# Performance work log

Measured on AMD Instinct MI355X. Metric: run time of the kernel, lower is better.

Reference implementation:

```python
import jax, jax.numpy as jnp
import numpy as np

HIDDEN = 128
EDGE = 64
EPS = 1e-5

def setup_inputs() -> dict:
    key = jax.random.key(0)
    ks = jax.random.split(key, 12)
    B, N, D = 8, 256, HIDDEN
    h = jax.random.normal(ks[0], (B, N, D), dtype=jnp.float32)
    edge_feats = jax.random.normal(ks[1], (B, N, N, 3), dtype=jnp.float32)
    adj_mask = jax.random.bernoulli(ks[2], 0.5, (B, N, N))
    s = lambda fan_in: 1.0 / np.sqrt(fan_in)
    W1 = jax.random.uniform(ks[3], (D + 3, EDGE), minval=-s(D + 3), maxval=s(D + 3))
    b1 = jnp.zeros((EDGE,), jnp.float32)
    W2 = jax.random.uniform(ks[4], (EDGE, D), minval=-s(EDGE), maxval=s(EDGE))
    b2 = jnp.zeros((D,), jnp.float32)
    U1 = jax.random.uniform(ks[5], (3 * D, D), minval=-s(3 * D), maxval=s(3 * D))
    b3 = jnp.zeros((D,), jnp.float32)
    U2 = jax.random.uniform(ks[6], (D, D), minval=-s(D), maxval=s(D))
    b4 = jnp.zeros((D,), jnp.float32)
    gamma = jnp.ones((D,), jnp.float32)
    beta = jnp.zeros((D,), jnp.float32)
    return {"h": h, "edge_feats": edge_feats, "adj_mask": adj_mask,
            "W1": W1, "b1": b1, "W2": W2, "b2": b2,
            "U1": U1, "b3": b3, "U2": U2, "b4": b4,
            "gamma": gamma, "beta": beta}

def reference(h, edge_feats, adj_mask, W1, b1, W2, b2, U1, b3, U2, b4, gamma, beta):
    B, N, D = h.shape
    # NOTE: torch does h.unsqueeze(2).expand(B,N,N,D): h_j[b,i,j,:] = h[b,i,:]
    h_j = jnp.broadcast_to(h[:, :, None, :], (B, N, N, D))
    gate_in = jnp.concatenate([h_j, edge_feats], axis=-1)          # (B,N,N,D+3)
    gates = jax.nn.sigmoid(jax.nn.relu(gate_in @ W1 + b1) @ W2 + b2)  # (B,N,N,D)
    mask_f = adj_mask.astype(h.dtype)[..., None]                    # (B,N,N,1)
    messages = gates * h_j * mask_f
    neighbor_count = jnp.clip(jnp.sum(mask_f, axis=2), 1.0)         # (B,N,1)
    agg_mean = jnp.sum(messages, axis=2) / neighbor_count           # (B,N,D)
    msgs_max = jnp.where(adj_mask[..., None], messages, -jnp.inf)
    agg_max = jnp.max(msgs_max, axis=2)
    agg_max = jnp.where(jnp.isinf(agg_max), 0.0, agg_max)
    upd_in = jnp.concatenate([h, agg_mean, agg_max], axis=-1)       # (B,N,3D)
    upd = jax.nn.relu(upd_in @ U1 + b3) @ U2 + b4
    x = h + upd
    mu = jnp.mean(x, axis=-1, keepdims=True)
    var = jnp.var(x, axis=-1, keepdims=True)
    return (x - mu) * jax.lax.rsqrt(var + EPS) * gamma + beta
```

## Files before the change

kernel.cpp:

```cpp
#include <hip/hip_runtime.h>
#include <hip/hip_bf16.h>
#include <math.h>

#define NN 256
#define DD 128
#define EE 64
#define APAD 392
#define RPAD 136

typedef __attribute__((ext_vector_type(8))) short short8;
typedef __attribute__((ext_vector_type(4))) float f32x4;

static __device__ __forceinline__ unsigned short f2bf(float f) {
    __hip_bfloat16 b = __float2bfloat16(f);
    return *reinterpret_cast<unsigned short*>(&b);
}

static __device__ __forceinline__ float sigm(float l) {
    return __fdividef(1.f, 1.f + __expf(-l));
}

static __device__ __forceinline__ short8 ldb(const float* __restrict__ B, int kbase, int d) {
    unsigned short tmp[8];
    #pragma unroll
    for (int j = 0; j < 8; ++j) tmp[j] = f2bf(B[(kbase + j) * DD + d]);
    return *(const short8*)tmp;
}

__global__ __launch_bounds__(256, 4)
void ecgc_gate(const float* __restrict__ h_g,
               const float* __restrict__ ef_g,
               const int*   __restrict__ mask_g,
               const float* __restrict__ W1_g,
               const float* __restrict__ b1_g,
               const float* __restrict__ W2_g,
               const float* __restrict__ b2_g,
               const float* __restrict__ U1_g,
               const float* __restrict__ U2_g,
               float*          __restrict__ aggf,
               unsigned short* __restrict__ u1t,
               unsigned short* __restrict__ u2t)
{
    const int bi   = blockIdx.x;
    const int t    = threadIdx.x;
    const int lane = t & 63;
    const int w    = t >> 6;
    const int m16  = lane & 15;
    const int quad = lane >> 4;

    __shared__ __align__(16) float sh_ef4[NN * 4];
    __shared__ __align__(16) float sh_q4[EE * 4];
    __shared__ float sh_basep[4 * EE];
    __shared__ float sh_w1e[3 * EE];
    __shared__ int   sh_jlist[NN], sh_wcnt[4], sh_cnt;

    if (t < 32) {
        const int flat = bi * 32 + t;
        if (flat < 384 * DD) {
            const int d = flat / 384, k = flat - d * 384;
            u1t[flat] = f2bf(U1_g[k * DD + d]);
        } else {
            const int f2i = flat - 384 * DD;
            const int d = f2i >> 7, k = f2i & 127;
            u2t[f2i] = f2bf(U2_g[k * DD + d]);
        }
    }

    {
        const float* efr = ef_g + (size_t)bi * NN * 3;
        sh_ef4[t * 4 + 0] = efr[t * 3 + 0];
        sh_ef4[t * 4 + 1] = efr[t * 3 + 1];
        sh_ef4[t * 4 + 2] = efr[t * 3 + 2];
        sh_ef4[t * 4 + 3] = 0.f;
    }
    if (t < 192) sh_w1e[t] = W1_g[(DD + (t >> 6)) * EE + (t & 63)];

    const int mk = (mask_g[bi * NN + t] != 0) ? 1 : 0;
    const unsigned long long bal = __ballot(mk);
    if (lane == 0) sh_wcnt[w] = __popcll(bal);
    const int pre = __popcll(bal & ((1ull << lane) - 1ull));

    {
        const int e = t & 63;
        float acc = 0.f;
        #pragma unroll 8
        for (int d = w * 32; d < w * 32 + 32; ++d)
            acc = fmaf(h_g[bi * DD + d], W1_g[d * EE + e], acc);
        sh_basep[w * EE + e] = acc;
    }

    const int dstripe = w * 32;
    short8 bfrag[2][2];
    float  nb2[2], hd2[2], flip[2];
    #pragma unroll
    for (int dt = 0; dt < 2; ++dt) {
        const int d = dstripe + 16 * dt + m16;
        nb2[dt] = b2_g[d];
        hd2[dt] = h_g[bi * DD + d];
        flip[dt] = (hd2[dt] >= 0.f) ? 1.f : -1.f;
        #pragma unroll
        for (int kh = 0; kh < 2; ++kh)
            bfrag[dt][kh] = ldb(W2_g, kh * 32 + quad * 8, d);
    }
    __syncthreads();

    {
        int wbase = 0;
        for (int ww = 0; ww < w; ++ww) wbase += sh_wcnt[ww];
        if (mk) sh_jlist[wbase + pre] = t;
        if (t == 0) sh_cnt = sh_wcnt[0] + sh_wcnt[1] + sh_wcnt[2] + sh_wcnt[3];
    }
    if (t < EE) {
        const float base = b1_g[t] + sh_basep[t] + sh_basep[EE + t] +
                           sh_basep[2 * EE + t] + sh_basep[3 * EE + t];
        sh_q4[t * 4 + 0] = base;
        sh_q4[t * 4 + 1] = sh_w1e[t];
        sh_q4[t * 4 + 2] = sh_w1e[EE + t];
        sh_q4[t * 4 + 3] = sh_w1e[2 * EE + t];
    }
    __syncthreads();

    f32x4 qa[8], qb[8];
    #pragma unroll
    for (int jj = 0; jj < 8; ++jj) {
        qa[jj] = *(const f32x4*)&sh_q4[(quad * 8 + jj) * 4];
        qb[jj] = *(const f32x4*)&sh_q4[(32 + quad * 8 + jj) * 4];
    }

    const int cnt = sh_cnt;
    const int njt = (cnt + 15) >> 4;

    float sum2[2] = {0.f, 0.f};
    float mm[2]   = {-3.0e38f, -3.0e38f};

    for (int jt = 0; jt < njt; ++jt) {
        const int row = jt * 16 + m16;
        int jl = sh_jlist[row];
        jl = (row < cnt) ? jl : 0;
        const float4 efv = *(const float4*)&sh_ef4[jl * 4];

        union { short8 s; __hip_bfloat162 h2[4]; } ua, ub;
        #pragma unroll
        for (int p = 0; p < 4; ++p) {
            const f32x4 qa0 = qa[2 * p], qa1 = qa[2 * p + 1];
            const f32x4 qb0 = qb[2 * p], qb1 = qb[2 * p + 1];
            float2 va, vb;
            va.x = fmaxf(fmaf(efv.z, qa0[3], fmaf(efv.y, qa0[2], fmaf(efv.x, qa0[1], qa0[0]))), 0.f);
            va.y = fmaxf(fmaf(efv.z, qa1[3], fmaf(efv.y, qa1[2], fmaf(efv.x, qa1[1], qa1[0]))), 0.f);
            vb.x = fmaxf(fmaf(efv.z, qb0[3], fmaf(efv.y, qb0[2], fmaf(efv.x, qb0[1], qb0[0]))), 0.f);
            vb.y = fmaxf(fmaf(efv.z, qb1[3], fmaf(efv.y, qb1[2], fmaf(efv.x, qb1[1], qb1[0]))), 0.f);
            ua.h2[p] = __float22bfloat162_rn(va);
            ub.h2[p] = __float22bfloat162_rn(vb);
        }

        const bool tail = (jt == njt - 1) && (cnt & 15);
        #pragma unroll
        for (int dt = 0; dt < 2; ++dt) {
            f32x4 acc = {nb2[dt], nb2[dt], nb2[dt], nb2[dt]};
            acc = __builtin_amdgcn_mfma_f32_16x16x32_bf16(ua.s, bfrag[dt][0], acc, 0, 0, 0);
            acc = __builtin_amdgcn_mfma_f32_16x16x32_bf16(ub.s, bfrag[dt][1], acc, 0, 0, 0);
            if (!tail) {
                #pragma unroll
                for (int r = 0; r < 4; ++r) {
                    const float l = acc[r];
                    mm[dt] = fmaxf(mm[dt], l * flip[dt]);
                    sum2[dt] += sigm(l);
                }
            } else {
                #pragma unroll
                for (int r = 0; r < 4; ++r) {
                    const bool v = (jt * 16 + quad * 4 + r) < cnt;
                    const float lx = v ? acc[r] : -3.0e38f;
                    const float pf = v ? acc[r] * flip[dt] : -3.0e38f;
                    mm[dt] = fmaxf(mm[dt], pf);
                    sum2[dt] += sigm(lx);
                }
            }
        }
    }

    #pragma unroll
    for (int dt = 0; dt < 2; ++dt) {
        float s = sum2[dt], M = mm[dt];
        s += __shfl_xor(s, 16, 64);  s += __shfl_xor(s, 32, 64);
        M  = fmaxf(M,  __shfl_xor(M, 16, 64));  M  = fmaxf(M,  __shfl_xor(M, 32, 64));
        if (quad == 0) {
            const int d = dstripe + 16 * dt + m16;
            const float hd = hd2[dt];
            float mean = 0.f, amax = 0.f;
            if (cnt > 0) {
                mean = hd * s * __fdividef(1.f, (float)cnt);
                amax = hd * sigm(flip[dt] * M);
            }
            aggf[bi * 256 + d]       = mean;
            aggf[bi * 256 + 128 + d] = amax;
        }
    }
}

__global__ __launch_bounds__(256, 2)
void ecgc_upd(const float* __restrict__ h_g,
              const float* __restrict__ aggf,
              const unsigned short* __restrict__ u1t,
              const unsigned short* __restrict__ u2t,
              const float* __restrict__ b3_g,
              const float* __restrict__ b4_g,
              const float* __restrict__ gam_g,
              const float* __restrict__ bet_g,
              float*       __restrict__ out_g)
{
    const int bi0  = blockIdx.x * 16;
    const int t    = threadIdx.x;
    const int lane = t & 63;
    const int w    = t >> 6;
    const int m16  = lane & 15;
    const int quad = lane >> 4;

    __shared__ __align__(16) unsigned short shA[16 * APAD];
    __shared__ __align__(16) unsigned short rbuf[16 * RPAD];
    __shared__ float sh_s[4 * 16], sh_s2[4 * 16], sh_mu[16], sh_rs[16];

    {
        const int row = t >> 4, q = t & 15;
        const float* hrow = h_g  + (size_t)(bi0 + row) * DD;
        const float* wrow = aggf + (size_t)(bi0 + row) * 256;
        unsigned short tmp[24];
        #pragma unroll
        for (int c = 0; c < 24; ++c) {
            const int col = q * 24 + c;
            float v;
            if (col < 128)      v = hrow[col];
            else if (col < 256) v = wrow[col - 128];
            else                v = wrow[col - 256 + 128];
            tmp[c] = f2bf(v);
        }
        #pragma unroll
        for (int s8 = 0; s8 < 3; ++s8)
            *(short8*)&shA[row * APAD + q * 24 + s8 * 8] = *(const short8*)&tmp[s8 * 8];
    }
    __syncthreads();

    const int dstripe = w * 32;

    f32x4 acc[2];
    #pragma unroll
    for (int dt = 0; dt < 2; ++dt) {
        const float bb = b3_g[dstripe + dt * 16 + m16];
        acc[dt] = (f32x4){bb, bb, bb, bb};
    }
    for (int kk = 0; kk < 12; ++kk) {
        const short8 a0 = *(const short8*)&shA[m16 * APAD + kk * 32 + quad * 8];
        #pragma unroll
        for (int dt = 0; dt < 2; ++dt) {
            const int d = dstripe + dt * 16 + m16;
            const short8 b = *(const short8*)&u1t[(size_t)d * 384 + kk * 32 + quad * 8];
            acc[dt] = __builtin_amdgcn_mfma_f32_16x16x32_bf16(a0, b, acc[dt], 0, 0, 0);
        }
    }

    #pragma unroll
    for (int dt = 0; dt < 2; ++dt) {
        const int d = dstripe + dt * 16 + m16;
        #pragma unroll
        for (int r = 0; r < 4; ++r) {
            const int ro = quad * 4 + r;
            rbuf[ro * RPAD + d] = f2bf(fmaxf(acc[dt][r], 0.f));
        }
    }
    __syncthreads();

    f32x4 acc2[2];
    #pragma unroll
    for (int dt = 0; dt < 2; ++dt) {
        const float bb = b4_g[dstripe + dt * 16 + m16];
        acc2[dt] = (f32x4){bb, bb, bb, bb};
    }
    for (int kk = 0; kk < 4; ++kk) {
        const short8 a0 = *(const short8*)&rbuf[m16 * RPAD + kk * 32 + quad * 8];
        #pragma unroll
        for (int dt = 0; dt < 2; ++dt) {
            const int d = dstripe + dt * 16 + m16;
            const short8 b = *(const short8*)&u2t[(size_t)d * 128 + kk * 32 + quad * 8];
            acc2[dt] = __builtin_amdgcn_mfma_f32_16x16x32_bf16(a0, b, acc2[dt], 0, 0, 0);
        }
    }

    float xv[2][4];
    #pragma unroll
    for (int dt = 0; dt < 2; ++dt) {
        const int d = dstripe + dt * 16 + m16;
        #pragma unroll
        for (int r = 0; r < 4; ++r) {
            const int ro = quad * 4 + r;
            xv[dt][r] = h_g[(size_t)(bi0 + ro) * DD + d] + acc2[dt][r];
        }
    }

    #pragma unroll
    for (int r = 0; r < 4; ++r) {
        float s  = xv[0][r] + xv[1][r];
        float s2 = xv[0][r] * xv[0][r] + xv[1][r] * xv[1][r];
        #pragma unroll
        for (int off = 1; off < 16; off <<= 1) {
            s  += __shfl_xor(s,  off, 64);
            s2 += __shfl_xor(s2, off, 64);
        }
        if (m16 == 0) {
            const int ro = quad * 4 + r;
            sh_s[w * 16 + ro]  = s;
            sh_s2[w * 16 + ro] = s2;
        }
    }
    __syncthreads();
    if (t < 16) {
        const float S  = sh_s[t]  + sh_s[16 + t]  + sh_s[32 + t]  + sh_s[48 + t];
        const float S2 = sh_s2[t] + sh_s2[16 + t] + sh_s2[32 + t] + sh_s2[48 + t];
        const float mu  = S * (1.f / 128.f);
        const float var = S2 * (1.f / 128.f) - mu * mu;
        sh_mu[t] = mu;
        sh_rs[t] = rsqrtf(var + 1e-5f);
    }
    __syncthreads();

    #pragma unroll
    for (int dt = 0; dt < 2; ++dt) {
        const int d = dstripe + dt * 16 + m16;
        const float ga = gam_g[d], be = bet_g[d];
        #pragma unroll
        for (int r = 0; r < 4; ++r) {
            const int ro = quad * 4 + r;
            out_g[(size_t)(bi0 + ro) * DD + d] =
                (xv[dt][r] - sh_mu[ro]) * sh_rs[ro] * ga + be;
        }
    }
}

extern "C" void kernel_launch(void* const* d_in, const int* in_sizes, int n_in,
                              void* d_out, int out_size, void* d_ws, size_t ws_size,
                              hipStream_t stream) {
    float* aggf = (float*)d_ws;
    unsigned short* u1t = (unsigned short*)((char*)d_ws + (size_t)2048 * 256 * 4);
    unsigned short* u2t = u1t + 384 * DD;
    ecgc_gate<<<8 * NN, 256, 0, stream>>>(
        (const float*)d_in[0],
        (const float*)d_in[1],
        (const int*)d_in[2],
        (const float*)d_in[3],
        (const float*)d_in[4],
        (const float*)d_in[5],
        (const float*)d_in[6],
        (const float*)d_in[7],
        (const float*)d_in[9],
        aggf, u1t, u2t);
    ecgc_upd<<<(8 * NN) / 16, 256, 0, stream>>>(
        (const float*)d_in[0],
        aggf, u1t, u2t,
        (const float*)d_in[8],
        (const float*)d_in[10],
        (const float*)d_in[11],
        (const float*)d_in[12],
        (float*)d_out);
}
```

Measured before the change: 121.7 us.

## Process two node rows per gate block to amortize setup and W2 fragment loads

Each gate block now handles two (batch,node) rows instead of one, halving the grid size. The per-block setup is shared across both rows: the W2 bf16 fragment loads, the W1 edge weights and the W1 column reads for the base projection. Edge features, masks and compacted neighbor lists are staged in LDS for both rows, and the neighbor loop then runs twice. The aim is to cut redundant global loads and launch overhead per row. In exchange it doubles LDS use per block and has fewer blocks to spread across CUs, which may reduce occupancy and parallelism.

```diff
diff --git a/kernel.cpp b/kernel.cpp
--- a/kernel.cpp
+++ b/kernel.cpp
@@ -41,21 +41,21 @@
                unsigned short* __restrict__ u1t,
                unsigned short* __restrict__ u2t)
 {
-    const int bi   = blockIdx.x;
+    const int bi0  = blockIdx.x * 2;
     const int t    = threadIdx.x;
     const int lane = t & 63;
     const int w    = t >> 6;
     const int m16  = lane & 15;
     const int quad = lane >> 4;
 
-    __shared__ __align__(16) float sh_ef4[NN * 4];
-    __shared__ __align__(16) float sh_q4[EE * 4];
-    __shared__ float sh_basep[4 * EE];
+    __shared__ __align__(16) float sh_ef4[2][NN * 4];
+    __shared__ __align__(16) float sh_q4[2][EE * 4];
+    __shared__ float sh_basep[2][4 * EE];
     __shared__ float sh_w1e[3 * EE];
-    __shared__ int   sh_jlist[NN], sh_wcnt[4], sh_cnt;
-
-    if (t < 32) {
-        const int flat = bi * 32 + t;
+    __shared__ int   sh_jlist[2][NN], sh_wcnt[2][4], sh_cnt[2];
+
+    if (t < 64) {
+        const int flat = blockIdx.x * 64 + t;
         if (flat < 384 * DD) {
             const int d = flat / 384, k = flat - d * 384;
             u1t[flat] = f2bf(U1_g[k * DD + d]);
@@ -66,134 +66,154 @@
         }
     }
 
-    {
-        const float* efr = ef_g + (size_t)bi * NN * 3;
-        sh_ef4[t * 4 + 0] = efr[t * 3 + 0];
-        sh_ef4[t * 4 + 1] = efr[t * 3 + 1];
-        sh_ef4[t * 4 + 2] = efr[t * 3 + 2];
-        sh_ef4[t * 4 + 3] = 0.f;
+    #pragma unroll
+    for (int p = 0; p < 2; ++p) {
+        const float* efr = ef_g + (size_t)(bi0 + p) * NN * 3;
+        sh_ef4[p][t * 4 + 0] = efr[t * 3 + 0];
+        sh_ef4[p][t * 4 + 1] = efr[t * 3 + 1];
+        sh_ef4[p][t * 4 + 2] = efr[t * 3 + 2];
+        sh_ef4[p][t * 4 + 3] = 0.f;
     }
     if (t < 192) sh_w1e[t] = W1_g[(DD + (t >> 6)) * EE + (t & 63)];
 
-    const int mk = (mask_g[bi * NN + t] != 0) ? 1 : 0;
-    const unsigned long long bal = __ballot(mk);
-    if (lane == 0) sh_wcnt[w] = __popcll(bal);
-    const int pre = __popcll(bal & ((1ull << lane) - 1ull));
+    int mk[2], pre[2];
+    #pragma unroll
+    for (int p = 0; p < 2; ++p) {
+        mk[p] = (mask_g[(bi0 + p) * NN + t] != 0) ? 1 : 0;
+        const unsigned long long bal = __ballot(mk[p]);
+        if (lane == 0) sh_wcnt[p][w] = __popcll(bal);
+        pre[p] = __popcll(bal & ((1ull << lane) - 1ull));
+    }
 
     {
         const int e = t & 63;
-        float acc = 0.f;
+        float a0 = 0.f, a1 = 0.f;
         #pragma unroll 8
-        for (int d = w * 32; d < w * 32 + 32; ++d)
-            acc = fmaf(h_g[bi * DD + d], W1_g[d * EE + e], acc);
-        sh_basep[w * EE + e] = acc;
+        for (int d = w * 32; d < w * 32 + 32; ++d) {
+            const float wv = W1_g[d * EE + e];
+            a0 = fmaf(h_g[bi0 * DD + d],       wv, a0);
+            a1 = fmaf(h_g[(bi0 + 1) * DD + d], wv, a1);
+        }
+        sh_basep[0][w * EE + e] = a0;
+        sh_basep[1][w * EE + e] = a1;
     }
 
     const int dstripe = w * 32;
     short8 bfrag[2][2];
-    float  nb2[2], hd2[2], flip[2];
+    float  nb2[2];
     #pragma unroll
     for (int dt = 0; dt < 2; ++dt) {
         const int d = dstripe + 16 * dt + m16;
         nb2[dt] = b2_g[d];
-        hd2[dt] = h_g[bi * DD + d];
-        flip[dt] = (hd2[dt] >= 0.f) ? 1.f : -1.f;
         #pragma unroll
         for (int kh = 0; kh < 2; ++kh)
             bfrag[dt][kh] = ldb(W2_g, kh * 32 + quad * 8, d);
     }
     __syncthreads();
 
-    {
+    #pragma unroll
+    for (int p = 0; p < 2; ++p) {
         int wbase = 0;
-        for (int ww = 0; ww < w; ++ww) wbase += sh_wcnt[ww];
-        if (mk) sh_jlist[wbase + pre] = t;
-        if (t == 0) sh_cnt = sh_wcnt[0] + sh_wcnt[1] + sh_wcnt[2] + sh_wcnt[3];
-    }
-    if (t < EE) {
-        const float base = b1_g[t] + sh_basep[t] + sh_basep[EE + t] +
-                           sh_basep[2 * EE + t] + sh_basep[3 * EE + t];
-        sh_q4[t * 4 + 0] = base;
-        sh_q4[t * 4 + 1] = sh_w1e[t];
-        sh_q4[t * 4 + 2] = sh_w1e[EE + t];
-        sh_q4[t * 4 + 3] = sh_w1e[2 * EE + t];
-    }
-    __syncthreads();
-
-    f32x4 qa[8], qb[8];
-    #pragma unroll
-    for (int jj = 0; jj < 8; ++jj) {
-        qa[jj] = *(const f32x4*)&sh_q4[(quad * 8 + jj) * 4];
-        qb[jj] = *(const f32x4*)&sh_q4[(32 + quad * 8 + jj) * 4];
-    }
-
-    const int cnt = sh_cnt;
-    const int njt = (cnt + 15) >> 4;
-
-    float sum2[2] = {0.f, 0.f};
-    float mm[2]   = {-3.0e38f, -3.0e38f};
-
-    for (int jt = 0; jt < njt; ++jt) {
-        const int row = jt * 16 + m16;
-        int jl = sh_jlist[row];
-        jl = (row < cnt) ? jl : 0;
-        const float4 efv = *(const float4*)&sh_ef4[jl * 4];
-
-        union { short8 s; __hip_bfloat162 h2[4]; } ua, ub;
-        #pragma unroll
-        for (int p = 0; p < 4; ++p) {
-            const f32x4 qa0 = qa[2 * p], qa1 = qa[2 * p + 1];
-            const f32x4 qb0 = qb[2 * p], qb1 = qb[2 * p + 1];
-            float2 va, vb;
-            va.x = fmaxf(fmaf(efv.z, qa0[3], fmaf(efv.y, qa0[2], fmaf(efv.x, qa0[1], qa0[0]))), 0.f);
-            va.y = fmaxf(fmaf(efv.z, qa1[3], fmaf(efv.y, qa1[2], fmaf(efv.x, qa1[1], qa1[0]))), 0.f);
-            vb.x = fmaxf(fmaf(efv.z, qb0[3], fmaf(efv.y, qb0[2], fmaf(efv.x, qb0[1], qb0[0]))), 0.f);
-            vb.y = fmaxf(fmaf(efv.z, qb1[3], fmaf(efv.y, qb1[2], fmaf(efv.x, qb1[1], qb1[0]))), 0.f);
-            ua.h2[p] = __float22bfloat162_rn(va);
-            ub.h2[p] = __float22bfloat162_rn(vb);
-        }
-
-        const bool tail = (jt == njt - 1) && (cnt & 15);
+        for (int ww = 0; ww < w; ++ww) wbase += sh_wcnt[p][ww];
+        if (mk[p]) sh_jlist[p][wbase + pre[p]] = t;
+        if (t == 0) sh_cnt[p] = sh_wcnt[p][0] + sh_wcnt[p][1] + sh_wcnt[p][2] + sh_wcnt[p][3];
+    }
+    if (t < 2 * EE) {
+        const int p = t >> 6, e = t & 63;
+        const float base = b1_g[e] + sh_basep[p][e] + sh_basep[p][EE + e] +
+                           sh_basep[p][2 * EE + e] + sh_basep[p][3 * EE + e];
+        sh_q4[p][e * 4 + 0] = base;
+        sh_q4[p][e * 4 + 1] = sh_w1e[e];
+        sh_q4[p][e * 4 + 2] = sh_w1e[EE + e];
+        sh_q4[p][e * 4 + 3] = sh_w1e[2 * EE + e];
+    }
+    __syncthreads();
+
+    for (int pass = 0; pass < 2; ++pass) {
+        const int bi = bi0 + pass;
+
+        f32x4 qa[8], qb[8];
+        #pragma unroll
+        for (int jj = 0; jj < 8; ++jj) {
+            qa[jj] = *(const f32x4*)&sh_q4[pass][(quad * 8 + jj) * 4];
+            qb[jj] = *(const f32x4*)&sh_q4[pass][(32 + quad * 8 + jj) * 4];
+        }
+
+        float hd2[2], flip[2];
         #pragma unroll
         for (int dt = 0; dt < 2; ++dt) {
-            f32x4 acc = {nb2[dt], nb2[dt], nb2[dt], nb2[dt]};
-            acc = __builtin_amdgcn_mfma_f32_16x16x32_bf16(ua.s, bfrag[dt][0], acc, 0, 0, 0);
-            acc = __builtin_amdgcn_mfma_f32_16x16x32_bf16(ub.s, bfrag[dt][1], acc, 0, 0, 0);
-            if (!tail) {
-                #pragma unroll
-                for (int r = 0; r < 4; ++r) {
-                    const float l = acc[r];
-                    mm[dt] = fmaxf(mm[dt], l * flip[dt]);
-                    sum2[dt] += sigm(l);
-                }
-            } else {
-                #pragma unroll
-                for (int r = 0; r < 4; ++r) {
-                    const bool v = (jt * 16 + quad * 4 + r) < cnt;
-                    const float lx = v ? acc[r] : -3.0e38f;
-                    const float pf = v ? acc[r] * flip[dt] : -3.0e38f;
-                    mm[dt] = fmaxf(mm[dt], pf);
-                    sum2[dt] += sigm(lx);
+            hd2[dt]  = h_g[bi * DD + dstripe + 16 * dt + m16];
+            flip[dt] = (hd2[dt] >= 0.f) ? 1.f : -1.f;
+        }
+
+        const int cnt = sh_cnt[pass];
+        const int njt = (cnt + 15) >> 4;
+
+        float sum2[2] = {0.f, 0.f};
+        float mm[2]   = {-3.0e38f, -3.0e38f};
+
+        for (int jt = 0; jt < njt; ++jt) {
+            const int row = jt * 16 + m16;
+            int jl = sh_jlist[pass][row];
+            jl = (row < cnt) ? jl : 0;
+            const float4 efv = *(const float4*)&sh_ef4[pass][jl * 4];
+
+            union { short8 s; __hip_bfloat162 h2[4]; } ua, ub;
+            #pragma unroll
+            for (int p = 0; p < 4; ++p) {
+                const f32x4 qa0 = qa[2 * p], qa1 = qa[2 * p + 1];
+                const f32x4 qb0 = qb[2 * p], qb1 = qb[2 * p + 1];
+                float2 va, vb;
+                va.x = fmaxf(fmaf(efv.z, qa0[3], fmaf(efv.y, qa0[2], fmaf(efv.x, qa0[1], qa0[0]))), 0.f);
+                va.y = fmaxf(fmaf(efv.z, qa1[3], fmaf(efv.y, qa1[2], fmaf(efv.x, qa1[1], qa1[0]))), 0.f);
+                vb.x = fmaxf(fmaf(efv.z, qb0[3], fmaf(efv.y, qb0[2], fmaf(efv.x, qb0[1], qb0[0]))), 0.f);
+                vb.y = fmaxf(fmaf(efv.z, qb1[3], fmaf(efv.y, qb1[2], fmaf(efv.x, qb1[1], qb1[0]))), 0.f);
+                ua.h2[p] = __float22bfloat162_rn(va);
+                ub.h2[p] = __float22bfloat162_rn(vb);
+            }
+
+            const bool tail = (jt == njt - 1) && (cnt & 15);
+            #pragma unroll
+            for (int dt = 0; dt < 2; ++dt) {
+                f32x4 acc = {nb2[dt], nb2[dt], nb2[dt], nb2[dt]};
+                acc = __builtin_amdgcn_mfma_f32_16x16x32_bf16(ua.s, bfrag[dt][0], acc, 0, 0, 0);
+                acc = __builtin_amdgcn_mfma_f32_16x16x32_bf16(ub.s, bfrag[dt][1], acc, 0, 0, 0);
+                if (!tail) {
+                    #pragma unroll
+                    for (int r = 0; r < 4; ++r) {
+                        const float l = acc[r];
+                        mm[dt] = fmaxf(mm[dt], l * flip[dt]);
+                        sum2[dt] += sigm(l);
+                    }
+                } else {
+                    #pragma unroll
+                    for (int r = 0; r < 4; ++r) {
+                        const bool v = (jt * 16 + quad * 4 + r) < cnt;
+                        const float lx = v ? acc[r] : -3.0e38f;
+                        const float pf = v ? acc[r] * flip[dt] : -3.0e38f;
+                        mm[dt] = fmaxf(mm[dt], pf);
+                        sum2[dt] += sigm(lx);
+                    }
                 }
             }
         }
-    }
-
-    #pragma unroll
-    for (int dt = 0; dt < 2; ++dt) {
-        float s = sum2[dt], M = mm[dt];
-        s += __shfl_xor(s, 16, 64);  s += __shfl_xor(s, 32, 64);
-        M  = fmaxf(M,  __shfl_xor(M, 16, 64));  M  = fmaxf(M,  __shfl_xor(M, 32, 64));
-        if (quad == 0) {
-            const int d = dstripe + 16 * dt + m16;
-            const float hd = hd2[dt];
-            float mean = 0.f, amax = 0.f;
-            if (cnt > 0) {
-                mean = hd * s * __fdividef(1.f, (float)cnt);
-                amax = hd * sigm(flip[dt] * M);
+
+        #pragma unroll
+        for (int dt = 0; dt < 2; ++dt) {
+            float s = sum2[dt], M = mm[dt];
+            s += __shfl_xor(s, 16, 64);  s += __shfl_xor(s, 32, 64);
+            M  = fmaxf(M,  __shfl_xor(M, 16, 64));  M  = fmaxf(M,  __shfl_xor(M, 32, 64));
+            if (quad == 0) {
+                const int d = dstripe + 16 * dt + m16;
+                const float hd = hd2[dt];
+                float mean = 0.f, amax = 0.f;
+                if (cnt > 0) {
+                    mean = hd * s * __fdividef(1.f, (float)cnt);
+                    amax = hd * sigm(flip[dt] * M);
+                }
+                aggf[bi * 256 + d]       = mean;
+                aggf[bi * 256 + 128 + d] = amax;
             }
-            aggf[bi * 256 + d]       = mean;
-            aggf[bi * 256 + 128 + d] = amax;
         }
     }
 }
@@ -341,7 +361,7 @@
     float* aggf = (float*)d_ws;
     unsigned short* u1t = (unsigned short*)((char*)d_ws + (size_t)2048 * 256 * 4);
     unsigned short* u2t = u1t + 384 * DD;
-    ecgc_gate<<<8 * NN, 256, 0, stream>>>(
+    ecgc_gate<<<(8 * NN) / 2, 256, 0, stream>>>(
         (const float*)d_in[0],
         (const float*)d_in[1],
         (const int*)d_in[2],
```

Result: no change. 123.9 us (+1.8%).
